# Kernel tuning notes

Hardware: AMD Instinct MI355X
Metric: run time of the kernel (lower is better)

## Reference

```python
import jax, jax.numpy as jnp
import numpy as np

B, T, N, E, F = 8, 12, 20000, 320000, 64  # batch, timedim, nodes, edges, gcn hidden


def setup_inputs() -> dict:
    key = jax.random.key(0)
    ks = jax.random.split(key, 8)
    x = jax.random.normal(ks[0], (B, T, N), dtype=jnp.float32)
    edge_src = jax.random.randint(ks[1], (E,), 0, N, dtype=jnp.int32)
    edge_dst = jax.random.randint(ks[2], (E,), 0, N, dtype=jnp.int32)
    # pre-normalized GCN adjacency values (spektral expects D^-1/2 (A+I) D^-1/2)
    edge_weight = jax.random.uniform(ks[3], (E,), dtype=jnp.float32)
    w_gcn = jax.random.normal(ks[4], (T, F), dtype=jnp.float32) * (1.0 / np.sqrt(T))
    b_gcn = jnp.zeros((F,), dtype=jnp.float32)
    w_dense = jax.random.normal(ks[5], (F, T), dtype=jnp.float32) * (1.0 / np.sqrt(F))
    b_dense = jnp.zeros((T,), dtype=jnp.float32)
    return {"x": x, "edge_weight": edge_weight, "w_gcn": w_gcn, "b_gcn": b_gcn,
            "w_dense": w_dense, "b_dense": b_dense,
            "edge_src": edge_src, "edge_dst": edge_dst}


def reference(x, edge_weight, w_gcn, b_gcn, w_dense, b_dense, edge_src, edge_dst):
    # x: [B, T, N] -> transpose to [B, N, T] (nodes x features), as in call()
    xt = jnp.transpose(x, (0, 2, 1))                      # [B, N, T]
    # GCNConv: relu(A @ (X @ W) + b)
    h = jnp.einsum("bnt,tf->bnf", xt, w_gcn)              # [B, N, F]
    msg = h[:, edge_src, :] * edge_weight[None, :, None]  # [B, E, F] gather * edge value
    agg = jnp.zeros_like(h).at[:, edge_dst, :].add(msg)   # scatter-add (SpMM)
    gcn = jax.nn.relu(agg + b_gcn)                        # [B, N, F]
    # SFDense: relu(gcn @ Wd + bd) -> [B, N, T]
    return jax.nn.relu(jnp.einsum("bnf,ft->bnt", gcn, w_dense) + b_dense)
```

## Files before the change

kernel.cpp:

```cpp
#include <hip/hip_runtime.h>

#define BB 8
#define TT 12
#define NN 20000
#define EE 320000
#define FF 64
#define NC 96
#define NU 48
#define CAP 64
#define POISON_I ((int)0xAAAAAAAAu)

#define PREP_BLOCKS ((NN + 255) / 256)
#define BUILD_BLOCKS ((EE + 255) / 256)

__device__ __forceinline__ unsigned int f2bf(float v) {
    unsigned int u = __float_as_uint(v);
    return (u + 0x7FFFu + ((u >> 16) & 1u)) >> 16;
}

__global__ __launch_bounds__(256) void prep_build_kernel(
        const float* __restrict__ x, unsigned int* __restrict__ xt,
        const int* __restrict__ esrc, const int* __restrict__ edst,
        const float* __restrict__ ew,
        int* __restrict__ cnt, int2* __restrict__ csrf) {
    if (blockIdx.x < PREP_BLOCKS) {
        int n = blockIdx.x * 256 + threadIdx.x;
        if (n >= NN) return;
        unsigned int* row = xt + (size_t)n * NU;
#pragma unroll
        for (int b = 0; b < BB; ++b) {
            float v[TT];
#pragma unroll
            for (int t = 0; t < TT; ++t)
                v[t] = x[((size_t)(b * TT + t)) * NN + n];
            unsigned int u[6];
#pragma unroll
            for (int j = 0; j < 6; ++j)
                u[j] = f2bf(v[2 * j]) | (f2bf(v[2 * j + 1]) << 16);
            uint2* o = reinterpret_cast<uint2*>(row + b * 6);
            o[0] = make_uint2(u[0], u[1]);
            o[1] = make_uint2(u[2], u[3]);
            o[2] = make_uint2(u[4], u[5]);
        }
    } else {
        int e = (blockIdx.x - PREP_BLOCKS) * 256 + threadIdx.x;
        if (e >= EE) return;
        int d = edst[e];
        int slot = atomicAdd(&cnt[d], 1) - POISON_I;
        if ((unsigned)slot < CAP)
            csrf[(size_t)d * CAP + slot] = make_int2(esrc[e], __float_as_int(ew[e]));
    }
}

__global__ __launch_bounds__(256) void agg_kernel(const unsigned int* __restrict__ xt,
                                                  const int* __restrict__ cnt,
                                                  const int2* __restrict__ csrf,
                                                  float* __restrict__ agg) {
    __shared__ float s_part[2][NC];
    int wid  = threadIdx.x >> 6;
    int lane = threadIdx.x & 63;
    int pair = wid >> 1;
    int half = wid & 1;
    int n = blockIdx.x * 2 + pair;

    int deg  = min(cnt[n] - POISON_I, CAP);
    int mid  = deg >> 1;
    int jbeg = half ? mid : 0;
    int jend = half ? deg : mid;

    const int2* row = csrf + (size_t)n * CAP;
    bool act = lane < NU;
    int li = act ? lane : (lane - 16);
    float a0 = 0.f, a1 = 0.f;
    int j = jbeg;
    for (; j + 4 <= jend; j += 4) {
        int2 e0 = row[j], e1 = row[j + 1], e2 = row[j + 2], e3 = row[j + 3];
        unsigned int v0 = xt[(size_t)e0.x * NU + li];
        unsigned int v1 = xt[(size_t)e1.x * NU + li];
        unsigned int v2 = xt[(size_t)e2.x * NU + li];
        unsigned int v3 = xt[(size_t)e3.x * NU + li];
        float w0 = __int_as_float(e0.y), w1 = __int_as_float(e1.y);
        float w2 = __int_as_float(e2.y), w3 = __int_as_float(e3.y);
        a0 = fmaf(w0, __uint_as_float(v0 << 16), a0);
        a1 = fmaf(w0, __uint_as_float(v0 & 0xFFFF0000u), a1);
        a0 = fmaf(w1, __uint_as_float(v1 << 16), a0);
        a1 = fmaf(w1, __uint_as_float(v1 & 0xFFFF0000u), a1);
        a0 = fmaf(w2, __uint_as_float(v2 << 16), a0);
        a1 = fmaf(w2, __uint_as_float(v2 & 0xFFFF0000u), a1);
        a0 = fmaf(w3, __uint_as_float(v3 << 16), a0);
        a1 = fmaf(w3, __uint_as_float(v3 & 0xFFFF0000u), a1);
    }
    for (; j < jend; ++j) {
        int2 e0 = row[j];
        unsigned int v0 = xt[(size_t)e0.x * NU + li];
        float w0 = __int_as_float(e0.y);
        a0 = fmaf(w0, __uint_as_float(v0 << 16), a0);
        a1 = fmaf(w0, __uint_as_float(v0 & 0xFFFF0000u), a1);
    }

    if (half == 1 && act) {
        float2* sp = reinterpret_cast<float2*>(&s_part[pair][2 * lane]);
        *sp = make_float2(a0, a1);
    }
    __syncthreads();
    if (half == 0 && act) {
        const float2 p = *reinterpret_cast<const float2*>(&s_part[pair][2 * lane]);
        float2* o = reinterpret_cast<float2*>(agg + (size_t)n * NC + 2 * lane);
        *o = make_float2(a0 + p.x, a1 + p.y);
    }
}

#define KN 2
__global__ __launch_bounds__(256) void dense_kernel(
        const float* __restrict__ agg,
        const float* __restrict__ wg,
        const float* __restrict__ bg,
        const float* __restrict__ wd,
        const float* __restrict__ bd,
        float* __restrict__ out) {
    __shared__ __align__(16) float s_wgT[FF * TT];
    __shared__ __align__(16) float s_wd[FF * TT];
    __shared__ float s_bg[FF];
    __shared__ float s_bd[TT];
    for (int i = threadIdx.x; i < FF * TT; i += 256) {
        int t = i / FF, f = i % FF;
        s_wgT[f * TT + t] = wg[i];
        s_wd[i] = wd[i];
    }
    if (threadIdx.x < FF) s_bg[threadIdx.x] = bg[threadIdx.x];
    if (threadIdx.x < TT) s_bd[threadIdx.x] = bd[threadIdx.x];
    __syncthreads();

    int b  = threadIdx.x >> 5;
    int nl = threadIdx.x & 31;
    int n0 = blockIdx.x * (32 * KN) + nl * KN;

    float yr[KN][TT];
    int nv = 0;
#pragma unroll
    for (int k = 0; k < KN; ++k) {
        int n = n0 + k;
        if (n < NN) {
            const float4* ar = reinterpret_cast<const float4*>(agg + (size_t)n * NC + b * TT);
            float4 a = ar[0], c = ar[1], d4 = ar[2];
            yr[k][0] = a.x;  yr[k][1] = a.y;  yr[k][2]  = a.z;  yr[k][3]  = a.w;
            yr[k][4] = c.x;  yr[k][5] = c.y;  yr[k][6]  = c.z;  yr[k][7]  = c.w;
            yr[k][8] = d4.x; yr[k][9] = d4.y; yr[k][10] = d4.z; yr[k][11] = d4.w;
            nv = k + 1;
        } else {
#pragma unroll
            for (int t = 0; t < TT; ++t) yr[k][t] = 0.f;
        }
    }

    float o[KN][TT];
#pragma unroll
    for (int k = 0; k < KN; ++k)
#pragma unroll
        for (int t = 0; t < TT; ++t) o[k][t] = s_bd[t];

#pragma unroll 8
    for (int f = 0; f < FF; ++f) {
        const float4* wgr = reinterpret_cast<const float4*>(&s_wgT[f * TT]);
        float4 g0 = wgr[0], g1 = wgr[1], g2 = wgr[2];
        const float4* wdr = reinterpret_cast<const float4*>(&s_wd[f * TT]);
        float4 d0 = wdr[0], d1 = wdr[1], d2 = wdr[2];
        float bgf = s_bg[f];
#pragma unroll
        for (int k = 0; k < KN; ++k) {
            float acc = bgf;
            acc += yr[k][0] * g0.x + yr[k][1] * g0.y + yr[k][2]  * g0.z + yr[k][3]  * g0.w;
            acc += yr[k][4] * g1.x + yr[k][5] * g1.y + yr[k][6]  * g1.z + yr[k][7]  * g1.w;
            acc += yr[k][8] * g2.x + yr[k][9] * g2.y + yr[k][10] * g2.z + yr[k][11] * g2.w;
            float g = fmaxf(acc, 0.f);
            o[k][0] += g * d0.x;  o[k][1] += g * d0.y;  o[k][2]  += g * d0.z;  o[k][3]  += g * d0.w;
            o[k][4] += g * d1.x;  o[k][5] += g * d1.y;  o[k][6]  += g * d1.z;  o[k][7]  += g * d1.w;
            o[k][8] += g * d2.x;  o[k][9] += g * d2.y;  o[k][10] += g * d2.z;  o[k][11] += g * d2.w;
        }
    }

#pragma unroll
    for (int k = 0; k < KN; ++k) {
        if (k >= nv) break;
        float4* op = reinterpret_cast<float4*>(out + ((size_t)b * NN + (n0 + k)) * TT);
        op[0] = make_float4(fmaxf(o[k][0], 0.f), fmaxf(o[k][1], 0.f),
                            fmaxf(o[k][2], 0.f), fmaxf(o[k][3], 0.f));
        op[1] = make_float4(fmaxf(o[k][4], 0.f), fmaxf(o[k][5], 0.f),
                            fmaxf(o[k][6], 0.f), fmaxf(o[k][7], 0.f));
        op[2] = make_float4(fmaxf(o[k][8], 0.f), fmaxf(o[k][9], 0.f),
                            fmaxf(o[k][10], 0.f), fmaxf(o[k][11], 0.f));
    }
}

extern "C" void kernel_launch(void* const* d_in, const int* in_sizes, int n_in,
                              void* d_out, int out_size, void* d_ws, size_t ws_size,
                              hipStream_t stream) {
    const float* x    = (const float*)d_in[0];
    const float* ew   = (const float*)d_in[1];
    const float* wg   = (const float*)d_in[2];
    const float* bg   = (const float*)d_in[3];
    const float* wd   = (const float*)d_in[4];
    const float* bd   = (const float*)d_in[5];
    const int*   esrc = (const int*)d_in[6];
    const int*   edst = (const int*)d_in[7];
    float* out = (float*)d_out;

    unsigned int* xt  = (unsigned int*)d_ws;
    float* agg  = (float*)(xt + (size_t)NN * NU);
    int2*  csrf = (int2*)(agg + (size_t)NN * NC);
    int*   cnt  = (int*)(csrf + (size_t)NN * CAP);

    prep_build_kernel<<<PREP_BLOCKS + BUILD_BLOCKS, 256, 0, stream>>>(
        x, xt, esrc, edst, ew, cnt, csrf);
    agg_kernel<<<NN / 2, 256, 0, stream>>>(xt, cnt, csrf, agg);
    dense_kernel<<<(NN + 32 * KN - 1) / (32 * KN), 256, 0, stream>>>(agg, wg, bg, wd, bd, out);
}
```

Before: 134.3 us.

## Fuse aggregation and dense stages into one kernel using shared-memory partials

Merges the gather-aggregation kernel and the two-layer dense kernel into a single kernel, so per-node aggregated features stay in shared memory instead of round-tripping through a global agg buffer. The dense part is remapped so that 16 lanes split the 64 hidden features for each (node, batch), followed by a shuffle-xor reduction. The weight tiles are padded to a stride of 13 to avoid LDS bank conflicts. In exchange, every block now reloads the weights into shared memory and the dense math is spread thinly, adding shuffle overhead across the 10000 blocks.

```diff
diff --git a/kernel.cpp b/kernel.cpp
--- a/kernel.cpp
+++ b/kernel.cpp
@@ -8,6 +8,7 @@
 #define NC 96
 #define NU 48
 #define CAP 64
+#define SWG 13
 #define POISON_I ((int)0xAAAAAAAAu)
 
 #define PREP_BLOCKS ((NN + 255) / 256)
@@ -52,143 +53,120 @@
     }
 }
 
-__global__ __launch_bounds__(256) void agg_kernel(const unsigned int* __restrict__ xt,
-                                                  const int* __restrict__ cnt,
-                                                  const int2* __restrict__ csrf,
-                                                  float* __restrict__ agg) {
-    __shared__ float s_part[2][NC];
-    int wid  = threadIdx.x >> 6;
-    int lane = threadIdx.x & 63;
-    int pair = wid >> 1;
-    int half = wid & 1;
-    int n = blockIdx.x * 2 + pair;
-
-    int deg  = min(cnt[n] - POISON_I, CAP);
-    int mid  = deg >> 1;
-    int jbeg = half ? mid : 0;
-    int jend = half ? deg : mid;
-
-    const int2* row = csrf + (size_t)n * CAP;
-    bool act = lane < NU;
-    int li = act ? lane : (lane - 16);
-    float a0 = 0.f, a1 = 0.f;
-    int j = jbeg;
-    for (; j + 4 <= jend; j += 4) {
-        int2 e0 = row[j], e1 = row[j + 1], e2 = row[j + 2], e3 = row[j + 3];
-        unsigned int v0 = xt[(size_t)e0.x * NU + li];
-        unsigned int v1 = xt[(size_t)e1.x * NU + li];
-        unsigned int v2 = xt[(size_t)e2.x * NU + li];
-        unsigned int v3 = xt[(size_t)e3.x * NU + li];
-        float w0 = __int_as_float(e0.y), w1 = __int_as_float(e1.y);
-        float w2 = __int_as_float(e2.y), w3 = __int_as_float(e3.y);
-        a0 = fmaf(w0, __uint_as_float(v0 << 16), a0);
-        a1 = fmaf(w0, __uint_as_float(v0 & 0xFFFF0000u), a1);
-        a0 = fmaf(w1, __uint_as_float(v1 << 16), a0);
-        a1 = fmaf(w1, __uint_as_float(v1 & 0xFFFF0000u), a1);
-        a0 = fmaf(w2, __uint_as_float(v2 << 16), a0);
-        a1 = fmaf(w2, __uint_as_float(v2 & 0xFFFF0000u), a1);
-        a0 = fmaf(w3, __uint_as_float(v3 << 16), a0);
-        a1 = fmaf(w3, __uint_as_float(v3 & 0xFFFF0000u), a1);
-    }
-    for (; j < jend; ++j) {
-        int2 e0 = row[j];
-        unsigned int v0 = xt[(size_t)e0.x * NU + li];
-        float w0 = __int_as_float(e0.y);
-        a0 = fmaf(w0, __uint_as_float(v0 << 16), a0);
-        a1 = fmaf(w0, __uint_as_float(v0 & 0xFFFF0000u), a1);
-    }
-
-    if (half == 1 && act) {
-        float2* sp = reinterpret_cast<float2*>(&s_part[pair][2 * lane]);
-        *sp = make_float2(a0, a1);
-    }
-    __syncthreads();
-    if (half == 0 && act) {
-        const float2 p = *reinterpret_cast<const float2*>(&s_part[pair][2 * lane]);
-        float2* o = reinterpret_cast<float2*>(agg + (size_t)n * NC + 2 * lane);
-        *o = make_float2(a0 + p.x, a1 + p.y);
-    }
-}
-
-#define KN 2
-__global__ __launch_bounds__(256) void dense_kernel(
-        const float* __restrict__ agg,
+__global__ __launch_bounds__(256) void agg_dense_kernel(
+        const unsigned int* __restrict__ xt,
+        const int* __restrict__ cnt,
+        const int2* __restrict__ csrf,
         const float* __restrict__ wg,
         const float* __restrict__ bg,
         const float* __restrict__ wd,
         const float* __restrict__ bd,
         float* __restrict__ out) {
-    __shared__ __align__(16) float s_wgT[FF * TT];
-    __shared__ __align__(16) float s_wd[FF * TT];
+    __shared__ __align__(16) float s_wgT[FF * SWG];
+    __shared__ __align__(16) float s_wd[FF * SWG];
     __shared__ float s_bg[FF];
     __shared__ float s_bd[TT];
+    __shared__ float s_part[2][2][NC];
+
     for (int i = threadIdx.x; i < FF * TT; i += 256) {
         int t = i / FF, f = i % FF;
-        s_wgT[f * TT + t] = wg[i];
-        s_wd[i] = wd[i];
+        s_wgT[f * SWG + t] = wg[i];
+        int f2 = i / TT, t2 = i % TT;
+        s_wd[f2 * SWG + t2] = wd[i];
     }
     if (threadIdx.x < FF) s_bg[threadIdx.x] = bg[threadIdx.x];
     if (threadIdx.x < TT) s_bd[threadIdx.x] = bd[threadIdx.x];
+
+    {
+        int wid  = threadIdx.x >> 6;
+        int lane = threadIdx.x & 63;
+        int pair = wid >> 1;
+        int half = wid & 1;
+        int n = blockIdx.x * 2 + pair;
+
+        int deg  = min(cnt[n] - POISON_I, CAP);
+        int mid  = deg >> 1;
+        int jbeg = half ? mid : 0;
+        int jend = half ? deg : mid;
+
+        const int2* row = csrf + (size_t)n * CAP;
+        bool act = lane < NU;
+        int li = act ? lane : (lane - 16);
+        float a0 = 0.f, a1 = 0.f;
+        int j = jbeg;
+        for (; j + 4 <= jend; j += 4) {
+            int2 e0 = row[j], e1 = row[j + 1], e2 = row[j + 2], e3 = row[j + 3];
+            unsigned int v0 = xt[(size_t)e0.x * NU + li];
+            unsigned int v1 = xt[(size_t)e1.x * NU + li];
+            unsigned int v2 = xt[(size_t)e2.x * NU + li];
+            unsigned int v3 = xt[(size_t)e3.x * NU + li];
+            float w0 = __int_as_float(e0.y), w1 = __int_as_float(e1.y);
+            float w2 = __int_as_float(e2.y), w3 = __int_as_float(e3.y);
+            a0 = fmaf(w0, __uint_as_float(v0 << 16), a0);
+            a1 = fmaf(w0, __uint_as_float(v0 & 0xFFFF0000u), a1);
+            a0 = fmaf(w1, __uint_as_float(v1 << 16), a0);
+            a1 = fmaf(w1, __uint_as_float(v1 & 0xFFFF0000u), a1);
+            a0 = fmaf(w2, __uint_as_float(v2 << 16), a0);
+            a1 = fmaf(w2, __uint_as_float(v2 & 0xFFFF0000u), a1);
+            a0 = fmaf(w3, __uint_as_float(v3 << 16), a0);
+            a1 = fmaf(w3, __uint_as_float(v3 & 0xFFFF0000u), a1);
+        }
+        for (; j < jend; ++j) {
+            int2 e0 = row[j];
+            unsigned int v0 = xt[(size_t)e0.x * NU + li];
+            float w0 = __int_as_float(e0.y);
+            a0 = fmaf(w0, __uint_as_float(v0 << 16), a0);
+            a1 = fmaf(w0, __uint_as_float(v0 & 0xFFFF0000u), a1);
+        }
+        if (act) {
+            float2* sp = reinterpret_cast<float2*>(&s_part[half][pair][2 * lane]);
+            *sp = make_float2(a0, a1);
+        }
+    }
     __syncthreads();
 
-    int b  = threadIdx.x >> 5;
-    int nl = threadIdx.x & 31;
-    int n0 = blockIdx.x * (32 * KN) + nl * KN;
+    {
+        int p   = threadIdx.x >> 7;
+        int b   = (threadIdx.x >> 4) & 7;
+        int l16 = threadIdx.x & 15;
+        int n = blockIdx.x * 2 + p;
 
-    float yr[KN][TT];
-    int nv = 0;
+        float y[TT];
 #pragma unroll
-    for (int k = 0; k < KN; ++k) {
-        int n = n0 + k;
-        if (n < NN) {
-            const float4* ar = reinterpret_cast<const float4*>(agg + (size_t)n * NC + b * TT);
-            float4 a = ar[0], c = ar[1], d4 = ar[2];
-            yr[k][0] = a.x;  yr[k][1] = a.y;  yr[k][2]  = a.z;  yr[k][3]  = a.w;
-            yr[k][4] = c.x;  yr[k][5] = c.y;  yr[k][6]  = c.z;  yr[k][7]  = c.w;
-            yr[k][8] = d4.x; yr[k][9] = d4.y; yr[k][10] = d4.z; yr[k][11] = d4.w;
-            nv = k + 1;
-        } else {
+        for (int t = 0; t < TT; ++t)
+            y[t] = s_part[0][p][b * TT + t] + s_part[1][p][b * TT + t];
+
+        float o[TT];
 #pragma unroll
-            for (int t = 0; t < TT; ++t) yr[k][t] = 0.f;
-        }
-    }
-
-    float o[KN][TT];
-#pragma unroll
-    for (int k = 0; k < KN; ++k)
-#pragma unroll
-        for (int t = 0; t < TT; ++t) o[k][t] = s_bd[t];
-
-#pragma unroll 8
-    for (int f = 0; f < FF; ++f) {
-        const float4* wgr = reinterpret_cast<const float4*>(&s_wgT[f * TT]);
-        float4 g0 = wgr[0], g1 = wgr[1], g2 = wgr[2];
-        const float4* wdr = reinterpret_cast<const float4*>(&s_wd[f * TT]);
-        float4 d0 = wdr[0], d1 = wdr[1], d2 = wdr[2];
-        float bgf = s_bg[f];
-#pragma unroll
-        for (int k = 0; k < KN; ++k) {
-            float acc = bgf;
-            acc += yr[k][0] * g0.x + yr[k][1] * g0.y + yr[k][2]  * g0.z + yr[k][3]  * g0.w;
-            acc += yr[k][4] * g1.x + yr[k][5] * g1.y + yr[k][6]  * g1.z + yr[k][7]  * g1.w;
-            acc += yr[k][8] * g2.x + yr[k][9] * g2.y + yr[k][10] * g2.z + yr[k][11] * g2.w;
-            float g = fmaxf(acc, 0.f);
-            o[k][0] += g * d0.x;  o[k][1] += g * d0.y;  o[k][2]  += g * d0.z;  o[k][3]  += g * d0.w;
-            o[k][4] += g * d1.x;  o[k][5] += g * d1.y;  o[k][6]  += g * d1.z;  o[k][7]  += g * d1.w;
-            o[k][8] += g * d2.x;  o[k][9] += g * d2.y;  o[k][10] += g * d2.z;  o[k][11] += g * d2.w;
-        }
-    }
+        for (int t = 0; t < TT; ++t) o[t] = 0.f;
 
 #pragma unroll
-    for (int k = 0; k < KN; ++k) {
-        if (k >= nv) break;
-        float4* op = reinterpret_cast<float4*>(out + ((size_t)b * NN + (n0 + k)) * TT);
-        op[0] = make_float4(fmaxf(o[k][0], 0.f), fmaxf(o[k][1], 0.f),
-                            fmaxf(o[k][2], 0.f), fmaxf(o[k][3], 0.f));
-        op[1] = make_float4(fmaxf(o[k][4], 0.f), fmaxf(o[k][5], 0.f),
-                            fmaxf(o[k][6], 0.f), fmaxf(o[k][7], 0.f));
-        op[2] = make_float4(fmaxf(o[k][8], 0.f), fmaxf(o[k][9], 0.f),
-                            fmaxf(o[k][10], 0.f), fmaxf(o[k][11], 0.f));
+        for (int q = 0; q < 4; ++q) {
+            int f = l16 * 4 + q;
+            const float* wgr = &s_wgT[f * SWG];
+            float acc = s_bg[f];
+#pragma unroll
+            for (int t = 0; t < TT; ++t) acc += y[t] * wgr[t];
+            float g = fmaxf(acc, 0.f);
+            const float* wdr = &s_wd[f * SWG];
+#pragma unroll
+            for (int t = 0; t < TT; ++t) o[t] += g * wdr[t];
+        }
+
+#pragma unroll
+        for (int off = 8; off > 0; off >>= 1)
+#pragma unroll
+            for (int t = 0; t < TT; ++t) o[t] += __shfl_xor(o[t], off);
+
+        if (l16 == 0) {
+            float r[TT];
+#pragma unroll
+            for (int t = 0; t < TT; ++t) r[t] = fmaxf(o[t] + s_bd[t], 0.f);
+            float4* op = reinterpret_cast<float4*>(out + ((size_t)b * NN + n) * TT);
+            op[0] = make_float4(r[0], r[1], r[2], r[3]);
+            op[1] = make_float4(r[4], r[5], r[6], r[7]);
+            op[2] = make_float4(r[8], r[9], r[10], r[11]);
+        }
     }
 }
 
@@ -206,12 +184,10 @@
     float* out = (float*)d_out;
 
     unsigned int* xt  = (unsigned int*)d_ws;
-    float* agg  = (float*)(xt + (size_t)NN * NU);
-    int2*  csrf = (int2*)(agg + (size_t)NN * NC);
+    int2*  csrf = (int2*)(xt + (size_t)NN * NU);
     int*   cnt  = (int*)(csrf + (size_t)NN * CAP);
 
     prep_build_kernel<<<PREP_BLOCKS + BUILD_BLOCKS, 256, 0, stream>>>(
         x, xt, esrc, edst, ew, cnt, csrf);
-    agg_kernel<<<NN / 2, 256, 0, stream>>>(xt, cnt, csrf, agg);
-    dense_kernel<<<(NN + 32 * KN - 1) / (32 * KN), 256, 0, stream>>>(agg, wg, bg, wd, bd, out);
+    agg_dense_kernel<<<NN / 2, 256, 0, stream>>>(xt, cnt, csrf, wg, bg, wd, bd, out);
 }
```

New measurement: 151.2 us. +12.6%, slower.
